# Optimization experiments

Measured on AMD Instinct MI355X. Metric: run time of the kernel, lower is better.

## Reference

```python
import jax, jax.numpy as jnp
import numpy as np

B, S, E, H, DH, W = 2, 4096, 1024, 16, 64, 512
NB = S // W          # number of query blocks
U = 2 * W            # key block = previous block + current block
INIT = 0.02


def setup_inputs() -> dict:
    key = jax.random.key(0)
    ks = jax.random.split(key, 6)
    x = jax.random.normal(ks[0], (B, S, E), jnp.float32)
    bias = jax.random.normal(ks[1], (H, W), jnp.float32)  # per-head alibi over rel. distance 0..W-1
    Wq = INIT * jax.random.normal(ks[2], (E, H, DH), jnp.float32)
    Wk = INIT * jax.random.normal(ks[3], (E, DH), jnp.float32)   # MQA: single shared K head
    Wv = INIT * jax.random.normal(ks[4], (E, DH), jnp.float32)   # MQA: single shared V head
    Wo = INIT * jax.random.normal(ks[5], (H, DH, E), jnp.float32)
    return {"x": x, "bias": bias, "Wq": Wq, "Wk": Wk, "Wv": Wv, "Wo": Wo}


def _sliding_window_attn(q, k, v, bias):
    # q: [B,S,H,DH]; k,v: [B,S,DH] (shared across heads); bias: [H,W]
    scale = 1.0 / np.sqrt(DH)
    qb = q.reshape(B, NB, W, H, DH)
    # pad one window of zeros in front so every query block sees a 'previous' block
    kp = jnp.pad(k, ((0, 0), (W, 0), (0, 0)))
    vp = jnp.pad(v, ((0, 0), (W, 0), (0, 0)))
    idx = jnp.arange(NB)[:, None] * W + jnp.arange(U)[None, :]  # [NB,U] into padded seq
    kb = kp[:, idx]  # [B,NB,U,DH]
    vb = vp[:, idx]  # [B,NB,U,DH]
    # scores over (query-in-block w, key-in-2W-block u)
    scores = jnp.einsum('bnwhd,bnud->bhnwu', qb, kb) * scale  # [B,H,NB,W,U]
    t = jnp.arange(W)
    u = jnp.arange(U)
    d = t[:, None] - u[None, :] + W                 # relative distance i-j, [W,U]
    rel_ok = (d >= 0) & (d < W)                     # causal + within window
    j_global = idx - W                              # global key position, [NB,U]
    valid = rel_ok[None, :, :] & (j_global >= 0)[:, None, :]  # [NB,W,U]
    bmat = bias[:, jnp.clip(d, 0, W - 1)]           # [H,W,U]
    scores = scores + bmat[None, :, None, :, :]
    neg = jnp.finfo(scores.dtype).min / 2
    scores = jnp.where(valid[None, None], scores, neg)
    p = jax.nn.softmax(scores, axis=-1)
    out = jnp.einsum('bhnwu,bnud->bnwhd', p, vb)    # [B,NB,W,H,DH]
    return out.reshape(B, S, H, DH)


def reference(x, bias, Wq, Wk, Wv, Wo):
    q = jnp.einsum('bse,ehd->bshd', x, Wq)
    k = jnp.einsum('bse,ed->bsd', x, Wk)
    v = jnp.einsum('bse,ed->bsd', x, Wv)
    attn = _sliding_window_attn(q, k, v, bias)
    return jnp.einsum('bshd,hde->bse', attn, Wo)
```

## Files before the change

kernel.cpp:

```cpp
#include <hip/hip_runtime.h>

#define Bx 2
#define Sx 4096
#define Ex 1024
#define Hx 16
#define DHx 64
#define Wwin 512

typedef unsigned short u16;
typedef unsigned int u32;
typedef __attribute__((ext_vector_type(8))) short bf16x8;
typedef __attribute__((ext_vector_type(4))) float f32x4;
typedef __attribute__((ext_vector_type(16))) float f32x16;
typedef __attribute__((ext_vector_type(4))) int i32x4;
typedef __attribute__((ext_vector_type(4))) unsigned short u16x4;

__device__ __forceinline__ u16 f2b(float f) {
  unsigned u = __builtin_bit_cast(unsigned, f);
  unsigned r = (u + 0x7FFFu + ((u >> 16) & 1u)) >> 16;
  return (u16)r;
}

__device__ __forceinline__ u32 cvt_pk_bf16(float lo, float hi) {
  u32 r;
  asm("v_cvt_pk_bf16_f32 %0, %1, %2" : "=v"(r) : "v"(lo), "v"(hi));
  return r;
}

__device__ __forceinline__ void gload_lds16(const void* g, void* l) {
  __builtin_amdgcn_global_load_lds(
      (const __attribute__((address_space(1))) void*)g,
      (__attribute__((address_space(3))) void*)l, 16, 0, 0);
}

__global__ __launch_bounds__(256) void cast_x_kernel(const float* __restrict__ x,
                                                     u16* __restrict__ xb) {
  long idx = ((long)blockIdx.x * 256 + threadIdx.x) * 4;
  float4 v = *(const float4*)(x + idx);
  u16x4 o;
  o[0] = f2b(v.x); o[1] = f2b(v.y); o[2] = f2b(v.z); o[3] = f2b(v.w);
  *(u16x4*)(xb + idx) = o;
}

__global__ __launch_bounds__(256) void pack_w_kernel(const float* __restrict__ Wq,
                                                     const float* __restrict__ Wk,
                                                     const float* __restrict__ Wv,
                                                     const float* __restrict__ Wo,
                                                     u16* __restrict__ wcat,
                                                     u16* __restrict__ wot) {
  int idx = blockIdx.x * 256 + threadIdx.x;
  if (idx < 1048576) {
    int e = idx >> 10, n = idx & 1023;
    wcat[n * 1024 + e] = f2b(Wq[idx]);
  } else if (idx < 1048576 + 65536) {
    int i2 = idx - 1048576;
    int e = i2 >> 6, d = i2 & 63;
    wcat[(1024 + d) * 1024 + e] = f2b(Wk[i2]);
  } else if (idx < 1048576 + 131072) {
    int i2 = idx - (1048576 + 65536);
    int e = i2 >> 6, d = i2 & 63;
    wcat[(1088 + d) * 1024 + e] = f2b(Wv[i2]);
  } else {
    int i2 = idx - (1048576 + 131072);
    int hd = i2 >> 10, e = i2 & 1023;
    wot[e * 1024 + hd] = f2b(Wo[i2]);
  }
}

template <typename OutT>
__global__ __launch_bounds__(256) void gemm_bt_kernel(const u16* __restrict__ A,
                                                      const u16* __restrict__ Bt,
                                                      OutT* __restrict__ C,
                                                      int M, int N, int K) {
  __shared__ u16 As[128 * 64];
  __shared__ u16 Bs[128 * 64];
  const int tid = threadIdx.x;
  const int lane = tid & 63, wave = tid >> 6;
  const int ll = lane & 15, gl = lane >> 4;
  const int wr = wave >> 1, wc = wave & 1;
  const long m0 = (long)blockIdx.x * 128;
  const long n0 = (long)blockIdx.y * 128;
  const int segrow = lane >> 3, cph = lane & 7;

  f32x4 acc[4][4] = {};

  for (int kb = 0; kb < K; kb += 64) {
    __syncthreads();
#pragma unroll
    for (int q = 0; q < 4; ++q) {
      int s = wave * 4 + q;
      int row = s * 8 + segrow;
      int clog = cph ^ (row & 7);
      gload_lds16(A + (m0 + row) * K + kb + clog * 8, (char*)As + s * 1024);
      gload_lds16(Bt + (n0 + row) * K + kb + clog * 8, (char*)Bs + s * 1024);
    }
    __syncthreads();
#pragma unroll
    for (int kx = 0; kx < 2; ++kx) {
      bf16x8 af[4], bfr[4];
#pragma unroll
      for (int rg = 0; rg < 4; ++rg) {
        int row = wr * 64 + rg * 16 + ll;
        int c = kx * 4 + gl;
        af[rg] = *(const bf16x8*)&As[row * 64 + ((c ^ (row & 7)) << 3)];
      }
#pragma unroll
      for (int cg = 0; cg < 4; ++cg) {
        int row = wc * 64 + cg * 16 + ll;
        int c = kx * 4 + gl;
        bfr[cg] = *(const bf16x8*)&Bs[row * 64 + ((c ^ (row & 7)) << 3)];
      }
#pragma unroll
      for (int rg = 0; rg < 4; ++rg)
#pragma unroll
        for (int cg = 0; cg < 4; ++cg)
          acc[rg][cg] = __builtin_amdgcn_mfma_f32_16x16x32_bf16(af[rg], bfr[cg],
                                                                acc[rg][cg], 0, 0, 0);
    }
  }
#pragma unroll
  for (int rg = 0; rg < 4; ++rg)
#pragma unroll
    for (int cg = 0; cg < 4; ++cg)
#pragma unroll
      for (int r = 0; r < 4; ++r) {
        long row = m0 + wr * 64 + rg * 16 + gl * 4 + r;
        long col = n0 + wc * 64 + cg * 16 + ll;
        if constexpr (sizeof(OutT) == 2)
          C[row * (long)N + col] = f2b(acc[rg][cg][r]);
        else
          C[row * (long)N + col] = acc[rg][cg][r];
      }
}

__global__ __launch_bounds__(256) void vt_transpose_kernel(const u16* __restrict__ qkvb,
                                                           u16* __restrict__ vt) {
  __shared__ u16 T[64 * 65];
  const int blk = blockIdx.x;
  const int b = blk >> 6;
  const int j0 = (blk & 63) * 64;
  const int tid = threadIdx.x;
#pragma unroll
  for (int rep = 0; rep < 16; ++rep) {
    int idx = rep * 256 + tid;
    int jj = idx >> 6, dd = idx & 63;
    T[dd * 65 + jj] = qkvb[((long)b * Sx + j0 + jj) * 1152 + 1088 + dd];
  }
  __syncthreads();
#pragma unroll
  for (int rep = 0; rep < 16; ++rep) {
    int idx = rep * 256 + tid;
    int dd = idx >> 6, jj = idx & 63;
    vt[((long)b * 64 + dd) * Sx + j0 + jj] = T[dd * 65 + jj];
  }
}

__global__ __launch_bounds__(256) void attn_kernel(const u16* __restrict__ qkv,
                                                   const u16* __restrict__ vt,
                                                   const float* __restrict__ bias,
                                                   u16* __restrict__ attnb) {
  __shared__ u16 Ks[2][64 * 64];
  __shared__ u16 Vts[2][64 * 64];
  __shared__ float bias2S[512];

  const int bid0 = blockIdx.x;
  const int bid = (bid0 & 7) * 128 + (bid0 >> 3);
  const int h = bid & 15;
  const int qt = (bid >> 4) & 31;
  const int b = bid >> 9;
  const int q0 = qt * 128;
  const long bS = (long)b * Sx;

  const int tid = threadIdx.x;
  const int lane = tid & 63, wave = tid >> 6;
  const int ql = lane & 31;
  const int hi = lane >> 5;
  const int wq0 = q0 + wave * 32;
  const int segrow = lane >> 3, cph = lane & 7;

  for (int i = tid; i < 512; i += 256)
    bias2S[i] = fmaf(bias[h * 512 + i], 1.4426950408889634f, -24.0f);

  const float C1 = 0.125f * 1.4426950408889634f;

  bf16x8 qf[4];
#pragma unroll
  for (int s = 0; s < 4; ++s)
    qf[s] = *(const bf16x8*)&qkv[(bS + wq0 + ql) * 1152 + h * 64 + s * 16 + hi * 8];

  bf16x8 vones;
#pragma unroll
  for (int i = 0; i < 8; ++i) vones[i] = (short)0x3F80;

  f32x16 oacc[2] = {};
  f32x16 lacc = {};

#define ATTN_STAGE(buf, kb)                                                     \
  {                                                                             \
    _Pragma("unroll") for (int q = 0; q < 2; ++q) {                             \
      int s = wave * 2 + q;                                                     \
      int rrow = s * 8 + segrow;                    \
      int clog = cph ^ (rrow & 7);                                              \
      gload_lds16(qkv + (bS + (kb) + rrow) * 1152 + 1024 + clog * 8,            \
                  (char*)&Ks[buf][0] + s * 1024);                               \
      gload_lds16(vt + ((long)b * 64 + rrow) * Sx + (kb) + clog * 8,            \
                  (char*)&Vts[buf][0] + s * 1024);                              \
    }                                                                           \
  }

  const int kb_start = (q0 > 511) ? (q0 - 512) : 0;
  const int kb_end = q0 + 64;
  ATTN_STAGE(0, kb_start);
  __syncthreads();
  int cur = 0;
  for (int kb = kb_start; kb <= kb_end; kb += 64) {
    if (kb + 64 <= kb_end) ATTN_STAGE(cur ^ 1, kb + 64);
    const bool active = (kb <= wq0 + 31) && (kb + 63 >= wq0 - 511);
    if (active) {
      f32x16 sacc[2] = {};
#pragma unroll
      for (int kblk = 0; kblk < 2; ++kblk) {
        int key = kblk * 32 + ql;
#pragma unroll
        for (int s = 0; s < 4; ++s) {
          int c = 2 * s + hi;
          bf16x8 kf = *(const bf16x8*)&Ks[cur][key * 64 + ((c ^ (key & 7)) << 3)];
          sacc[kblk] = __builtin_amdgcn_mfma_f32_32x32x16_bf16(kf, qf[s],
                                                               sacc[kblk], 0, 0, 0);
        }
      }
      const int dbase = wq0 + ql - kb - 4 * hi;
      const bool full = (kb - wq0 >= -480) && (kb - wq0 <= -64);
      if (full) {
        const float* bpz = bias2S + dbase - 63;
#pragma unroll
        for (int kblk = 0; kblk < 2; ++kblk)
#pragma unroll
          for (int r = 0; r < 16; ++r) {
            const int off = kblk * 32 + (r & 3) + 8 * (r >> 2);
            sacc[kblk][r] = __builtin_exp2f(fmaf(sacc[kblk][r], C1, bpz[63 - off]));
          }
      } else {
#pragma unroll
        for (int kblk = 0; kblk < 2; ++kblk)
#pragma unroll
          for (int r = 0; r < 16; ++r) {
            const int off = kblk * 32 + (r & 3) + 8 * (r >> 2);
            int d = dbase - off;
            int dc = d < 0 ? 0 : (d > 511 ? 511 : d);
            float p = __builtin_exp2f(fmaf(sacc[kblk][r], C1, bias2S[dc]));
            sacc[kblk][r] = ((unsigned)d < 512u) ? p : 0.0f;
          }
      }
#pragma unroll
      for (int s = 0; s < 4; ++s) {
        const int kblk = s >> 1;
        const int m0 = 2 * (s & 1);
        u32 a0 = cvt_pk_bf16(sacc[kblk][4 * m0 + 0], sacc[kblk][4 * m0 + 1]);
        u32 a1 = cvt_pk_bf16(sacc[kblk][4 * m0 + 2], sacc[kblk][4 * m0 + 3]);
        u32 b0 = cvt_pk_bf16(sacc[kblk][4 * m0 + 4], sacc[kblk][4 * m0 + 5]);
        u32 b1 = cvt_pk_bf16(sacc[kblk][4 * m0 + 6], sacc[kblk][4 * m0 + 7]);
        asm("v_permlane32_swap_b32 %0, %1" : "+v"(a0), "+v"(b0));
        asm("v_permlane32_swap_b32 %0, %1" : "+v"(a1), "+v"(b1));
        i32x4 t;
        t.x = (int)a0; t.y = (int)a1; t.z = (int)b0; t.w = (int)b1;
        bf16x8 pa = __builtin_bit_cast(bf16x8, t);
        lacc = __builtin_amdgcn_mfma_f32_32x32x16_bf16(pa, vones, lacc, 0, 0, 0);
#pragma unroll
        for (int dhblk = 0; dhblk < 2; ++dhblk) {
          int dh = dhblk * 32 + ql;
          int c = 2 * s + hi;
          bf16x8 vf = *(const bf16x8*)&Vts[cur][dh * 64 + ((c ^ (dh & 7)) << 3)];
          oacc[dhblk] = __builtin_amdgcn_mfma_f32_32x32x16_bf16(pa, vf,
                                                                oacc[dhblk], 0, 0, 0);
        }
      }
    }
    __syncthreads();
    cur ^= 1;
  }
#undef ATTN_STAGE
#pragma unroll
  for (int r = 0; r < 16; ++r) {
    const int q = (r & 3) + 8 * (r >> 2) + 4 * hi;
    float inv = 1.0f / lacc[r];
    long row = (bS + wq0 + q) * 1024 + h * 64;
#pragma unroll
    for (int dhblk = 0; dhblk < 2; ++dhblk)
      attnb[row + dhblk * 32 + ql] = f2b(oacc[dhblk][r] * inv);
  }
}

extern "C" void kernel_launch(void* const* d_in, const int* in_sizes, int n_in,
                              void* d_out, int out_size, void* d_ws, size_t ws_size,
                              hipStream_t stream) {
  const float* x    = (const float*)d_in[0];
  const float* bias = (const float*)d_in[1];
  const float* Wq   = (const float*)d_in[2];
  const float* Wk   = (const float*)d_in[3];
  const float* Wv   = (const float*)d_in[4];
  const float* Wo   = (const float*)d_in[5];
  float* out = (float*)d_out;

  u16* xb    = (u16*)d_ws;
  u16* wcat  = xb    + (size_t)8192 * 1024;
  u16* wot   = wcat  + (size_t)1152 * 1024;
  u16* qkvb  = wot   + (size_t)1024 * 1024;
  u16* vtb   = qkvb  + (size_t)8192 * 1152;
  u16* attnb = xb;

  cast_x_kernel<<<8192, 256, 0, stream>>>(x, xb);
  pack_w_kernel<<<8704, 256, 0, stream>>>(Wq, Wk, Wv, Wo, wcat, wot);
  gemm_bt_kernel<u16><<<dim3(64, 9), 256, 0, stream>>>(xb, wcat, qkvb, 8192, 1152, 1024);
  vt_transpose_kernel<<<128, 256, 0, stream>>>(qkvb, vtb);
  attn_kernel<<<1024, 256, 0, stream>>>(qkvb, vtb, bias, attnb);
  gemm_bt_kernel<float><<<dim3(64, 8), 256, 0, stream>>>(attnb, wot, out, 8192, 1024, 1024);
}
```

Baseline: 208.9 us.

## Enlarge attention query tile to 256 rows and tile-transpose weight packing

The attention kernel now runs 512-thread blocks covering 256 queries (8 waves) instead of 128, so each staged K/V tile in shared memory is reused by twice as many waves and fewer blocks re-read overlapping key windows. Each wave now loads one K and one V row-group per stage instead of two. Separately, the weight packing kernel replaces scattered per-element transposed writes with a 64x64 shared-memory tile transpose using float4 reads and vector writes. In exchange, the attention grid has half as many blocks, which lowers parallelism, and waves in a block cover a wider key range, so more stages are partly idle for some waves.

```diff
diff --git a/kernel.cpp b/kernel.cpp
--- a/kernel.cpp
+++ b/kernel.cpp
@@ -48,22 +48,29 @@
                                                      const float* __restrict__ Wo,
                                                      u16* __restrict__ wcat,
                                                      u16* __restrict__ wot) {
-  int idx = blockIdx.x * 256 + threadIdx.x;
-  if (idx < 1048576) {
-    int e = idx >> 10, n = idx & 1023;
-    wcat[n * 1024 + e] = f2b(Wq[idx]);
-  } else if (idx < 1048576 + 65536) {
-    int i2 = idx - 1048576;
-    int e = i2 >> 6, d = i2 & 63;
-    wcat[(1024 + d) * 1024 + e] = f2b(Wk[i2]);
-  } else if (idx < 1048576 + 131072) {
-    int i2 = idx - (1048576 + 65536);
-    int e = i2 >> 6, d = i2 & 63;
-    wcat[(1088 + d) * 1024 + e] = f2b(Wv[i2]);
-  } else {
-    int i2 = idx - (1048576 + 131072);
-    int hd = i2 >> 10, e = i2 & 1023;
-    wot[e * 1024 + hd] = f2b(Wo[i2]);
+  __shared__ u16 T[64][65];
+  const int blk = blockIdx.x;
+  const float* S; u16* D; int Cld, r0, c0;
+  if (blk < 256)      { S = Wq; D = wcat;               Cld = 1024; r0 = (blk >> 4) * 64;        c0 = (blk & 15) * 64; }
+  else if (blk < 272) { S = Wk; D = wcat + 1024 * 1024; Cld = 64;   r0 = (blk - 256) * 64;       c0 = 0; }
+  else if (blk < 288) { S = Wv; D = wcat + 1088 * 1024; Cld = 64;   r0 = (blk - 272) * 64;       c0 = 0; }
+  else                { S = Wo; D = wot;                Cld = 1024; r0 = ((blk - 288) >> 4) * 64; c0 = ((blk - 288) & 15) * 64; }
+  const int t = threadIdx.x;
+  const int tr = t >> 4, tc = (t & 15) * 4;
+#pragma unroll
+  for (int p = 0; p < 4; ++p) {
+    int r = p * 16 + tr;
+    float4 v = *(const float4*)&S[(long)(r0 + r) * Cld + c0 + tc];
+    T[tc + 0][r] = f2b(v.x); T[tc + 1][r] = f2b(v.y);
+    T[tc + 2][r] = f2b(v.z); T[tc + 3][r] = f2b(v.w);
+  }
+  __syncthreads();
+#pragma unroll
+  for (int p = 0; p < 4; ++p) {
+    int c = p * 16 + tr;
+    u16x4 o;
+    o[0] = T[c][tc]; o[1] = T[c][tc + 1]; o[2] = T[c][tc + 2]; o[3] = T[c][tc + 3];
+    *(u16x4*)&D[(long)(c0 + c) * 1024 + r0 + tc] = o;
   }
 }
 
@@ -155,7 +162,7 @@
   }
 }
 
-__global__ __launch_bounds__(256) void attn_kernel(const u16* __restrict__ qkv,
+__global__ __launch_bounds__(512) void attn_kernel(const u16* __restrict__ qkv,
                                                    const u16* __restrict__ vt,
                                                    const float* __restrict__ bias,
                                                    u16* __restrict__ attnb) {
@@ -164,11 +171,11 @@
   __shared__ float bias2S[512];
 
   const int bid0 = blockIdx.x;
-  const int bid = (bid0 & 7) * 128 + (bid0 >> 3);
+  const int bid = (bid0 & 7) * 64 + (bid0 >> 3);
   const int h = bid & 15;
-  const int qt = (bid >> 4) & 31;
-  const int b = bid >> 9;
-  const int q0 = qt * 128;
+  const int qt = (bid >> 4) & 15;
+  const int b = bid >> 8;
+  const int q0 = qt * 256;
   const long bS = (long)b * Sx;
 
   const int tid = threadIdx.x;
@@ -178,8 +185,8 @@
   const int wq0 = q0 + wave * 32;
   const int segrow = lane >> 3, cph = lane & 7;
 
-  for (int i = tid; i < 512; i += 256)
-    bias2S[i] = fmaf(bias[h * 512 + i], 1.4426950408889634f, -24.0f);
+  if (tid < 512)
+    bias2S[tid] = fmaf(bias[h * 512 + tid], 1.4426950408889634f, -24.0f);
 
   const float C1 = 0.125f * 1.4426950408889634f;
 
@@ -197,19 +204,17 @@
 
 #define ATTN_STAGE(buf, kb)                                                     \
   {                                                                             \
-    _Pragma("unroll") for (int q = 0; q < 2; ++q) {                             \
-      int s = wave * 2 + q;                                                     \
-      int rrow = s * 8 + segrow;                    \
-      int clog = cph ^ (rrow & 7);                                              \
-      gload_lds16(qkv + (bS + (kb) + rrow) * 1152 + 1024 + clog * 8,            \
-                  (char*)&Ks[buf][0] + s * 1024);                               \
-      gload_lds16(vt + ((long)b * 64 + rrow) * Sx + (kb) + clog * 8,            \
-                  (char*)&Vts[buf][0] + s * 1024);                              \
-    }                                                                           \
+    int s = wave;                 \
+    int rrow = s * 8 + segrow;                      \
+    int clog = cph ^ (rrow & 7);                                                \
+    gload_lds16(qkv + (bS + (kb) + rrow) * 1152 + 1024 + clog * 8,              \
+                (char*)&Ks[buf][0] + s * 1024);                                 \
+    gload_lds16(vt + ((long)b * 64 + rrow) * Sx + (kb) + clog * 8,              \
+                (char*)&Vts[buf][0] + s * 1024);                                \
   }
 
   const int kb_start = (q0 > 511) ? (q0 - 512) : 0;
-  const int kb_end = q0 + 64;
+  const int kb_end = q0 + 192;
   ATTN_STAGE(0, kb_start);
   __syncthreads();
   int cur = 0;
@@ -310,9 +315,9 @@
   u16* attnb = xb;
 
   cast_x_kernel<<<8192, 256, 0, stream>>>(x, xb);
-  pack_w_kernel<<<8704, 256, 0, stream>>>(Wq, Wk, Wv, Wo, wcat, wot);
+  pack_w_kernel<<<544, 256, 0, stream>>>(Wq, Wk, Wv, Wo, wcat, wot);
   gemm_bt_kernel<u16><<<dim3(64, 9), 256, 0, stream>>>(xb, wcat, qkvb, 8192, 1152, 1024);
   vt_transpose_kernel<<<128, 256, 0, stream>>>(qkvb, vtb);
-  attn_kernel<<<1024, 256, 0, stream>>>(qkvb, vtb, bias, attnb);
+  attn_kernel<<<512, 512, 0, stream>>>(qkvb, vtb, bias, attnb);
   gemm_bt_kernel<float><<<dim3(64, 8), 256, 0, stream>>>(attnb, wot, out, 8192, 1024, 1024);
 }
```

Result: no change. 206.5 us (-1.2%).
